# Kernel tuning notes

Measured on AMD Instinct MI355X. Metric: run time of the kernel, lower is better.

## Reference

```python
import jax, jax.numpy as jnp
import numpy as np

D = 512          # d_model
DS = 32          # d_state
EXPAND = 2
HEADDIM = 64
R = 4            # mimo_rank
DIN = EXPAND * D             # 1024 inner dim
H = DIN // HEADDIM           # 16 heads
DFF = ((int(D * 8 / 3) + 7) // 8) * 8  # 1368 SwiGLU hidden
CHUNK = max(1, 64 // R)      # 16
BATCH, SEQ = 4, 512


def setup_inputs() -> dict:
    key = jax.random.key(0)
    ks = jax.random.split(key, 12)
    def w(k, shape, fan):
        return jax.random.normal(k, shape, jnp.float32) / np.float32(np.sqrt(fan))
    return {
        "x": jax.random.normal(ks[0], (BATCH, SEQ, D), jnp.float32),
        "mask": jnp.ones((BATCH, SEQ), jnp.float32),
        "norm1_w": jnp.ones((D,), jnp.float32),
        "norm2_w": jnp.ones((D,), jnp.float32),
        "Wz": w(ks[1], (D, DIN), D),
        "Wx": w(ks[2], (D, DIN), D),
        "Wb": w(ks[3], (D, H * R * DS), D),
        "Wc": w(ks[4], (D, H * R * DS), D),
        "Wdt": w(ks[5], (D, H), D),
        "dt_bias": jnp.zeros((H,), jnp.float32),
        "A_log": jnp.log(jnp.arange(1, H + 1, dtype=jnp.float32)),
        "D_skip": jnp.ones((H,), jnp.float32),
        "Wout": w(ks[6], (DIN, D), DIN),
        "w1": w(ks[7], (D, DFF), D),
        "w2": w(ks[8], (DFF, D), DFF),
        "w3": w(ks[9], (D, DFF), D),
    }


def rmsnorm(x, wgt, eps=1e-6):
    rms = jnp.sqrt(jnp.mean(x * x, axis=-1, keepdims=True) + eps)
    return x / rms * wgt


def ssm_mixer(x, Wz, Wx, Wb, Wc, Wdt, dt_bias, A_log, D_skip, Wout):
    # x: [B, S, D] (already masked)
    B, S, _ = x.shape
    pad = (CHUNK - S % CHUNK) % CHUNK
    if pad > 0:
        x = jnp.pad(x, ((0, 0), (0, pad), (0, 0)))
    Sp = x.shape[1]
    z = x @ Wz                                        # [B,Sp,DIN] gate
    u = (x @ Wx).reshape(B, Sp, H, HEADDIM)           # [B,Sp,H,P]
    Bm = (x @ Wb).reshape(B, Sp, H, R, DS)            # [B,Sp,H,R,N]
    Cm = (x @ Wc).reshape(B, Sp, H, R, DS)
    dt = jax.nn.softplus(x @ Wdt + dt_bias)           # [B,Sp,H]
    a = jnp.exp(dt * (-jnp.exp(A_log)))               # per-step decay [B,Sp,H]
    ud = u * dt[..., None]                            # discretized input

    def step(h, inp):
        a_t, B_t, C_t, ud_t = inp                     # [B,H], [B,H,R,N], [B,H,R,N], [B,H,P]
        h = a_t[:, :, None, None, None] * h + jnp.einsum('bhrn,bhp->bhrnp', B_t, ud_t)
        y = jnp.einsum('bhrn,bhrnp->bhp', C_t, h)
        return h, y

    h0 = jnp.zeros((B, H, R, DS, HEADDIM), x.dtype)
    xs = (a.swapaxes(0, 1), Bm.swapaxes(0, 1), Cm.swapaxes(0, 1), ud.swapaxes(0, 1))
    _, ys = jax.lax.scan(step, h0, xs)                # ys: [Sp,B,H,P]
    y = ys.swapaxes(0, 1) + u * D_skip[None, None, :, None]
    y = y.reshape(B, Sp, DIN) * jax.nn.silu(z)
    y = y @ Wout                                      # [B,Sp,D]
    return y[:, :S]


def reference(x, mask, norm1_w, norm2_w, Wz, Wx, Wb, Wc, Wdt, dt_bias,
              A_log, D_skip, Wout, w1, w2, w3):
    m = mask[..., None]
    xn = rmsnorm(x, norm1_w) * m
    y = ssm_mixer(xn, Wz, Wx, Wb, Wc, Wdt, dt_bias, A_log, D_skip, Wout) * m
    x = x + y
    xn2 = rmsnorm(x, norm2_w)
    x = x + (jax.nn.silu(xn2 @ w1) * (xn2 @ w3)) @ w2
    return x * m
```

## Files before the change

kernel.cpp:

```cpp
#include <hip/hip_runtime.h>
#include <hip/hip_bf16.h>
#include <math.h>

#define Bn 4
#define Sn 512
#define Dn 512
#define DINn 1024
#define Hn 16
#define Pn 64
#define RNn 128
#define DFFn 1368
#define KP2 1408
#define BSn (Bn*Sn)
#define CH 64
#define NCH (Sn/CH)
#define PSTR 6144
#define FPAD 2816
#define NSCAN (Bn*NCH*Hn)
#define NRMS 512

typedef __attribute__((ext_vector_type(8))) short short8;
typedef __attribute__((ext_vector_type(4))) float f32x4;
typedef __attribute__((ext_vector_type(4))) short short4v;

static __device__ __forceinline__ float bf2f(__hip_bfloat16 v){return __bfloat162float(v);}
static __device__ __forceinline__ __hip_bfloat16 f2bf(float v){return __float2bfloat16(v);}
static __device__ __forceinline__ short f2bfs(float v){ __hip_bfloat16 b=f2bf(v); short s; __builtin_memcpy(&s,&b,2); return s; }
static __device__ __forceinline__ float bfs2f(short s){ __hip_bfloat16 b; __builtin_memcpy(&b,&s,2); return bf2f(b); }

static __device__ __forceinline__ int xcd_swz(int bid, int q) {
  return (bid & 7) * q + (bid >> 3);
}

typedef const __attribute__((address_space(1))) unsigned int* gas1_u32p;
typedef __attribute__((address_space(3))) unsigned int* gas3_u32p;
static __device__ __forceinline__ void gl_lds16(const void* g, void* l) {
  __builtin_amdgcn_global_load_lds((gas1_u32p)g, (gas3_u32p)l, 16, 0, 0);
}

struct T8 {
  const float* src[8];
  const float* svec[8];
  __hip_bfloat16* dst[8];
  int Rr[8], Cc[8], RrPad[8], CcPad[8], gw[8];
  int start[9];
};

static __device__ __forceinline__ void transpose_tile(const T8& d, int bid, int t,
                                                      float (*tile)[65]) {
  int i = 0;
#pragma unroll
  for (int k = 1; k < 8; ++k) if (bid >= d.start[k]) i = k;
  int rel = bid - d.start[i];
  int gx = rel % d.gw[i], gy = rel / d.gw[i];
  const float* in = d.src[i];
  const float* sv = d.svec[i];
  __hip_bfloat16* out = d.dst[i];
  int Rr = d.Rr[i], Cc = d.Cc[i], RrPad = d.RrPad[i], CcPad = d.CcPad[i];
  int tx = t & 15, ty = t >> 4;
#pragma unroll
  for (int i4 = 0; i4 < 4; ++i4) {
    int r = gy * 64 + ty + i4 * 16;
    int c0 = gx * 64 + tx * 4;
    f32x4 v = (f32x4){0.f, 0.f, 0.f, 0.f};
    if (r < Rr && c0 + 3 < Cc) v = *(const f32x4*)(in + (size_t)r * Cc + c0);
    tile[ty + i4 * 16][tx * 4 + 0] = v[0];
    tile[ty + i4 * 16][tx * 4 + 1] = v[1];
    tile[ty + i4 * 16][tx * 4 + 2] = v[2];
    tile[ty + i4 * 16][tx * 4 + 3] = v[3];
  }
  __syncthreads();
#pragma unroll
  for (int i4 = 0; i4 < 4; ++i4) {
    int r2 = gx * 64 + ty + i4 * 16;
    int c2 = gy * 64 + tx * 4;
    if (r2 < CcPad && c2 + 3 < RrPad) {
      int k = ty + i4 * 16;
      float s0 = sv ? sv[c2 + 0] : 1.f;
      float s1 = sv ? sv[c2 + 1] : 1.f;
      float s2 = sv ? sv[c2 + 2] : 1.f;
      float s3 = sv ? sv[c2 + 3] : 1.f;
      short4v o;
      o.x = f2bfs(tile[tx * 4 + 0][k] * s0);
      o.y = f2bfs(tile[tx * 4 + 1][k] * s1);
      o.z = f2bfs(tile[tx * 4 + 2][k] * s2);
      o.w = f2bfs(tile[tx * 4 + 3][k] * s3);
      *(short4v*)((short*)out + (size_t)r2 * RrPad + c2) = o;
    }
  }
}

__global__ __launch_bounds__(256) void prep_kernel(
    T8 d, const float* __restrict__ x, const float* __restrict__ w,
    const float* __restrict__ mask, const float* __restrict__ Wdt,
    const float* __restrict__ dtb, const float* __restrict__ Alog,
    __hip_bfloat16* __restrict__ outb, float* __restrict__ dt,
    float* __restrict__ la, float* __restrict__ rs, int tstart) {
  __shared__ __align__(16) char smem[40960];
  int bid = blockIdx.x, t = threadIdx.x;
  if (bid < tstart) {
    transpose_tile(d, bid, t, (float(*)[65])smem);
  } else if (bid - tstart < NRMS) {
    float* wdtS = (float*)smem;
    float* xsS  = (float*)(smem + 32768);
#pragma unroll
    for (int i = 0; i < 8; ++i) {
      int idx = t + i * 256;
      *(f32x4*)&wdtS[idx * 4] = *(const f32x4*)&Wdt[idx * 4];
    }
    __syncthreads();
    int wv = t >> 6, lane = t & 63;
    int row = (bid - tstart) * 4 + wv;
    const float* xr = x + (size_t)row * Dn;
    f32x4 v0 = *(const f32x4*)(xr + lane * 4);
    f32x4 v1 = *(const f32x4*)(xr + 256 + lane * 4);
    float ss = v0[0]*v0[0] + v0[1]*v0[1] + v0[2]*v0[2] + v0[3]*v0[3]
             + v1[0]*v1[0] + v1[1]*v1[1] + v1[2]*v1[2] + v1[3]*v1[3];
#pragma unroll
    for (int o = 32; o > 0; o >>= 1) ss += __shfl_xor(ss, o);
    float sc = rsqrtf(ss * (1.f / Dn) + 1e-6f) * mask[row];
    f32x4 w0 = *(const f32x4*)(w + lane * 4);
    f32x4 w1 = *(const f32x4*)(w + 256 + lane * 4);
    f32x4 o0, o1;
#pragma unroll
    for (int j = 0; j < 4; ++j) { o0[j] = v0[j] * sc * w0[j]; o1[j] = v1[j] * sc * w1[j]; }
    short4v b0, b1;
    b0.x = f2bfs(o0[0]); b0.y = f2bfs(o0[1]); b0.z = f2bfs(o0[2]); b0.w = f2bfs(o0[3]);
    b1.x = f2bfs(o1[0]); b1.y = f2bfs(o1[1]); b1.z = f2bfs(o1[2]); b1.w = f2bfs(o1[3]);
    *(short4v*)((short*)outb + (size_t)row * Dn + lane * 4) = b0;
    *(short4v*)((short*)outb + (size_t)row * Dn + 256 + lane * 4) = b1;
    *(f32x4*)&xsS[wv * 512 + lane * 4] = o0;
    *(f32x4*)&xsS[wv * 512 + 256 + lane * 4] = o1;
    int h = lane >> 2, j = lane & 3;
    float s = 0.f;
#pragma unroll 8
    for (int kk = 0; kk < 128; ++kk) {
      int k = j + kk * 4;
      s = fmaf(xsS[wv * 512 + k], wdtS[k * Hn + h], s);
    }
    s += __shfl_down(s, 2, 4);
    s += __shfl_down(s, 1, 4);
    if (j == 0) {
      float v = s + dtb[h];
      float sp = (v > 20.f) ? v : log1pf(expf(v));
      float Ah = expf(Alog[h]);
      dt[(size_t)row * Hn + h] = sp;
      la[(size_t)row * Hn + h] = -Ah * sp;
    }
  } else {
    *(f32x4*)&rs[t * 8]     = (f32x4){0.f, 0.f, 0.f, 0.f};
    *(f32x4*)&rs[t * 8 + 4] = (f32x4){0.f, 0.f, 0.f, 0.f};
  }
}

__global__ __launch_bounds__(256) void gemm_kernel(
    const __hip_bfloat16* __restrict__ A, const __hip_bfloat16* __restrict__ BT,
    __hip_bfloat16* __restrict__ C, int M, int N, int K) {
  __shared__ short As[2][4096];
  __shared__ short Bs[2][4096];
  int mblocks = M >> 7;
  int wg = xcd_swz(blockIdx.x, (int)gridDim.x >> 3);
  int m0 = (wg % mblocks) * 128, n0 = (wg / mblocks) * 128;
  int t = threadIdx.x;
  int lane = t & 63, wv = t >> 6;
  int wm = (wv & 1) * 64, wn = (wv >> 1) * 64;
  f32x4 acc[4][4];
#pragma unroll
  for (int i = 0; i < 4; ++i)
#pragma unroll
    for (int j = 0; j < 4; ++j) acc[i][j] = (f32x4){0.f, 0.f, 0.f, 0.f};
  const short* Ag = (const short*)A;
  const short* Bg = (const short*)BT;
  int r0 = t >> 2, p = t & 3;
  int q0 = (p - (r0 >> 1)) & 3;
  int r1 = r0 + 64;
  int q1 = (p - (r1 >> 1)) & 3;
  const short* Asrc0 = Ag + (size_t)(m0 + r0) * K + 8 * q0;
  const short* Asrc1 = Ag + (size_t)(m0 + r1) * K + 8 * q1;
  const short* Bsrc0 = Bg + (size_t)(n0 + r0) * K + 8 * q0;
  const short* Bsrc1 = Bg + (size_t)(n0 + r1) * K + 8 * q1;
  int fr = lane & 15, fq = lane >> 4;
  int kTiles = K >> 5;
  auto stage = [&](int buf, int k0) {
    gl_lds16(Asrc0 + k0, &As[buf][wv * 512]);
    gl_lds16(Asrc1 + k0, &As[buf][2048 + wv * 512]);
    gl_lds16(Bsrc0 + k0, &Bs[buf][wv * 512]);
    gl_lds16(Bsrc1 + k0, &Bs[buf][2048 + wv * 512]);
  };
  auto domfma = [&](int buf) {
    short8 af[4], bfr[4];
#pragma unroll
    for (int i = 0; i < 4; ++i) {
      int rr = wm + i * 16 + fr;
      af[i] = *(const short8*)&As[buf][rr * 32 + (((rr >> 1) + fq) & 3) * 8];
    }
#pragma unroll
    for (int i = 0; i < 4; ++i) {
      int rr = wn + i * 16 + fr;
      bfr[i] = *(const short8*)&Bs[buf][rr * 32 + (((rr >> 1) + fq) & 3) * 8];
    }
#pragma unroll
    for (int mi = 0; mi < 4; ++mi)
#pragma unroll
      for (int ni = 0; ni < 4; ++ni)
        acc[mi][ni] = __builtin_amdgcn_mfma_f32_16x16x32_bf16(af[mi], bfr[ni], acc[mi][ni], 0, 0, 0);
  };
  stage(0, 0);
  for (int kt = 0; kt < kTiles; ++kt) {
    int buf = kt & 1;
    __syncthreads();
    if (kt + 1 < kTiles) stage(buf ^ 1, (kt + 1) << 5);
    domfma(buf);
  }
  int fq4 = (lane >> 4) * 4;
#pragma unroll
  for (int mi = 0; mi < 4; ++mi)
#pragma unroll
    for (int ni = 0; ni < 4; ++ni) {
      int col = n0 + wn + ni * 16 + fr;
      if (col < N) {
        int rowb = m0 + wm + mi * 16 + fq4;
#pragma unroll
        for (int r = 0; r < 4; ++r)
          C[(size_t)(rowb + r) * N + col] = f2bf(acc[mi][ni][r]);
      }
    }
}

template <int MODE>
__global__ __launch_bounds__(256) void gemm64_ep_kernel(
    const __hip_bfloat16* __restrict__ A, const __hip_bfloat16* __restrict__ BT,
    const float* __restrict__ aux, const float* __restrict__ mask,
    float* __restrict__ out, __hip_bfloat16* __restrict__ outb,
    float* __restrict__ rs, int M, int N, int K) {
  __shared__ short As[2][64][72];
  __shared__ short Bs[2][64][72];
  int mblocks = M >> 6;
  int wg = xcd_swz(blockIdx.x, (int)gridDim.x >> 3);
  int m0 = (wg % mblocks) * 64, n0 = (wg / mblocks) * 64;
  int t = threadIdx.x;
  int lane = t & 63, wv = t >> 6;
  int wm = (wv & 1) * 32, wn = (wv >> 1) * 32;
  f32x4 acc[2][2];
#pragma unroll
  for (int i = 0; i < 2; ++i)
#pragma unroll
    for (int j = 0; j < 2; ++j) acc[i][j] = (f32x4){0.f, 0.f, 0.f, 0.f};
  const short* Ag = (const short*)A;
  const short* Bg = (const short*)BT;
  int sr = t >> 2;
  int sc = (t & 3) * 16;
  const short* Ap = Ag + (size_t)(m0 + sr) * K + sc;
  const short* Bp = Bg + (size_t)(n0 + sr) * K + sc;
  int fr = lane & 15, fq = (lane >> 4) * 8;
  int kTiles = K >> 6;
  short8 a0A = 0, a1A = 0, b0A = 0, b1A = 0;
  short8 a0B = 0, a1B = 0, b0B = 0, b1B = 0;
  auto loadA = [&](int k0) {
    a0A = *(const short8*)(Ap + k0);
    a1A = *(const short8*)(Ap + k0 + 8);
    b0A = *(const short8*)(Bp + k0);
    b1A = *(const short8*)(Bp + k0 + 8);
  };
  auto loadB = [&](int k0) {
    a0B = *(const short8*)(Ap + k0);
    a1B = *(const short8*)(Ap + k0 + 8);
    b0B = *(const short8*)(Bp + k0);
    b1B = *(const short8*)(Bp + k0 + 8);
  };
  auto storeA = [&](int buf) {
    *(short8*)&As[buf][sr][sc] = a0A;
    *(short8*)&As[buf][sr][sc + 8] = a1A;
    *(short8*)&Bs[buf][sr][sc] = b0A;
    *(short8*)&Bs[buf][sr][sc + 8] = b1A;
  };
  auto storeB = [&](int buf) {
    *(short8*)&As[buf][sr][sc] = a0B;
    *(short8*)&As[buf][sr][sc + 8] = a1B;
    *(short8*)&Bs[buf][sr][sc] = b0B;
    *(short8*)&Bs[buf][sr][sc + 8] = b1B;
  };
  auto mfma = [&](int buf) {
#pragma unroll
    for (int kk = 0; kk < 2; ++kk) {
      short8 af[2], bfr[2];
#pragma unroll
      for (int i = 0; i < 2; ++i) af[i] = *(const short8*)&As[buf][wm + i * 16 + fr][kk * 32 + fq];
#pragma unroll
      for (int i = 0; i < 2; ++i) bfr[i] = *(const short8*)&Bs[buf][wn + i * 16 + fr][kk * 32 + fq];
#pragma unroll
      for (int mi = 0; mi < 2; ++mi)
#pragma unroll
        for (int ni = 0; ni < 2; ++ni)
          acc[mi][ni] = __builtin_amdgcn_mfma_f32_16x16x32_bf16(af[mi], bfr[ni], acc[mi][ni], 0, 0, 0);
    }
  };
  loadA(0);
  storeA(0);
  loadA(64);
  __syncthreads();
  for (int kt = 0; kt < kTiles; kt += 2) {
    storeA(1);
    if (kt + 2 < kTiles) loadB((kt + 2) << 6);
    mfma(0);
    __syncthreads();
    if (kt + 2 < kTiles) storeB(0);
    if (kt + 3 < kTiles) loadA((kt + 3) << 6);
    mfma(1);
    __syncthreads();
  }
  int fq4 = (lane >> 4) * 4;
  float rsum[2][4];
#pragma unroll
  for (int mi = 0; mi < 2; ++mi)
#pragma unroll
    for (int r = 0; r < 4; ++r) rsum[mi][r] = 0.f;
#pragma unroll
  for (int mi = 0; mi < 2; ++mi)
#pragma unroll
    for (int ni = 0; ni < 2; ++ni) {
      int col = n0 + wn + ni * 16 + fr;
#pragma unroll
      for (int r = 0; r < 4; ++r) {
        int row = m0 + wm + mi * 16 + fq4 + r;
        float m = mask[row];
        size_t a = (size_t)row * N + col;
        float v = acc[mi][ni][r];
        if (MODE == 1) {
          float ov = aux[a] + v * m;
          out[a] = ov;
          outb[a] = f2bf(ov);
          rsum[mi][r] += ov * ov;
        } else {
          out[a] = (aux[a] + v) * m;
        }
      }
    }
  if (MODE == 1) {
#pragma unroll
    for (int mi = 0; mi < 2; ++mi)
#pragma unroll
      for (int r = 0; r < 4; ++r) {
        float s = rsum[mi][r];
#pragma unroll
        for (int o = 8; o > 0; o >>= 1) s += __shfl_xor(s, o);
        if ((lane & 15) == 0) {
          int row = m0 + wm + mi * 16 + fq4 + r;
          atomicAdd(&rs[row], s);
        }
      }
  }
}

__global__ __launch_bounds__(256) void gemm64g_kernel(
    const __hip_bfloat16* __restrict__ A, const float* __restrict__ rs,
    const __hip_bfloat16* __restrict__ BT, __hip_bfloat16* __restrict__ G,
    int M, int K) {
  __shared__ short As[2][64][72];
  __shared__ short B1s[2][64][72];
  __shared__ short B3s[2][64][72];
  __shared__ float ssc[64];
  int mblocks = M >> 6;
  int wg = xcd_swz(blockIdx.x, (int)gridDim.x >> 3);
  int m0 = (wg % mblocks) * 64, n0 = (wg / mblocks) * 64;
  int t = threadIdx.x;
  int lane = t & 63, wv = t >> 6;
  int wm = (wv & 1) * 32, wn = (wv >> 1) * 32;
  f32x4 acc1[2][2], acc3[2][2];
#pragma unroll
  for (int i = 0; i < 2; ++i)
#pragma unroll
    for (int j = 0; j < 2; ++j) {
      acc1[i][j] = (f32x4){0.f, 0.f, 0.f, 0.f};
      acc3[i][j] = (f32x4){0.f, 0.f, 0.f, 0.f};
    }
  const short* Ag = (const short*)A;
  const short* Bg = (const short*)BT;
  int sr = t >> 2;
  int sc = (t & 3) * 16;
  const short* Ap  = Ag + (size_t)(m0 + sr) * K + sc;
  const short* B1p = Bg + (size_t)(n0 + sr) * K + sc;
  const short* B3p = Bg + (size_t)(KP2 + n0 + sr) * K + sc;
  int fr = lane & 15, fq = (lane >> 4) * 8;
  int kTiles = K >> 6;
  if (t < 64) ssc[t] = rsqrtf(rs[m0 + t] * (1.f / Dn) + 1e-6f);
  short8 a0A = 0, a1A = 0, c0A = 0, c1A = 0, d0A = 0, d1A = 0;
  short8 a0B = 0, a1B = 0, c0B = 0, c1B = 0, d0B = 0, d1B = 0;
  auto loadA = [&](int k0) {
    a0A = *(const short8*)(Ap + k0);
    a1A = *(const short8*)(Ap + k0 + 8);
    c0A = *(const short8*)(B1p + k0);
    c1A = *(const short8*)(B1p + k0 + 8);
    d0A = *(const short8*)(B3p + k0);
    d1A = *(const short8*)(B3p + k0 + 8);
  };
  auto loadB = [&](int k0) {
    a0B = *(const short8*)(Ap + k0);
    a1B = *(const short8*)(Ap + k0 + 8);
    c0B = *(const short8*)(B1p + k0);
    c1B = *(const short8*)(B1p + k0 + 8);
    d0B = *(const short8*)(B3p + k0);
    d1B = *(const short8*)(B3p + k0 + 8);
  };
  auto storeA = [&](int buf) {
    *(short8*)&As[buf][sr][sc] = a0A;
    *(short8*)&As[buf][sr][sc + 8] = a1A;
    *(short8*)&B1s[buf][sr][sc] = c0A;
    *(short8*)&B1s[buf][sr][sc + 8] = c1A;
    *(short8*)&B3s[buf][sr][sc] = d0A;
    *(short8*)&B3s[buf][sr][sc + 8] = d1A;
  };
  auto storeB = [&](int buf) {
    *(short8*)&As[buf][sr][sc] = a0B;
    *(short8*)&As[buf][sr][sc + 8] = a1B;
    *(short8*)&B1s[buf][sr][sc] = c0B;
    *(short8*)&B1s[buf][sr][sc + 8] = c1B;
    *(short8*)&B3s[buf][sr][sc] = d0B;
    *(short8*)&B3s[buf][sr][sc + 8] = d1B;
  };
  auto mfma = [&](int buf) {
#pragma unroll
    for (int kk = 0; kk < 2; ++kk) {
      short8 af[2], b1f[2], b3f[2];
#pragma unroll
      for (int i = 0; i < 2; ++i) af[i]  = *(const short8*)&As[buf][wm + i * 16 + fr][kk * 32 + fq];
#pragma unroll
      for (int i = 0; i < 2; ++i) b1f[i] = *(const short8*)&B1s[buf][wn + i * 16 + fr][kk * 32 + fq];
#pragma unroll
      for (int i = 0; i < 2; ++i) b3f[i] = *(const short8*)&B3s[buf][wn + i * 16 + fr][kk * 32 + fq];
#pragma unroll
      for (int mi = 0; mi < 2; ++mi)
#pragma unroll
        for (int ni = 0; ni < 2; ++ni) {
          acc1[mi][ni] = __builtin_amdgcn_mfma_f32_16x16x32_bf16(af[mi], b1f[ni], acc1[mi][ni], 0, 0, 0);
          acc3[mi][ni] = __builtin_amdgcn_mfma_f32_16x16x32_bf16(af[mi], b3f[ni], acc3[mi][ni], 0, 0, 0);
        }
    }
  };
  loadA(0);
  storeA(0);
  loadA(64);
  __syncthreads();
  for (int kt = 0; kt < kTiles; kt += 2) {
    storeA(1);
    if (kt + 2 < kTiles) loadB((kt + 2) << 6);
    mfma(0);
    __syncthreads();
    if (kt + 2 < kTiles) storeB(0);
    if (kt + 3 < kTiles) loadA((kt + 3) << 6);
    mfma(1);
    __syncthreads();
  }
  int fq4 = (lane >> 4) * 4;
#pragma unroll
  for (int mi = 0; mi < 2; ++mi)
#pragma unroll
    for (int ni = 0; ni < 2; ++ni) {
      int col = n0 + wn + ni * 16 + fr;
#pragma unroll
      for (int r = 0; r < 4; ++r) {
        int rloc = wm + mi * 16 + fq4 + r;
        float scl = ssc[rloc];
        float h1v = acc1[mi][ni][r] * scl;
        float sil = h1v / (1.f + __expf(-h1v));
        float g = sil * (acc3[mi][ni][r] * scl);
        G[(size_t)(m0 + rloc) * KP2 + col] = f2bf(g);
      }
    }
}

__global__ __launch_bounds__(256) void chunk_state_kernel(
    const __hip_bfloat16* __restrict__ P, const float* __restrict__ dt,
    const float* __restrict__ la, __hip_bfloat16* __restrict__ Sbuf,
    float* __restrict__ ecL) {
  int id = blockIdx.x;
  int h = id & 15, c = (id >> 4) & 7, b = id >> 7;
  int t = threadIdx.x, lane = t & 63, wv = t >> 6;
  __shared__ __align__(16) char smem[45824];
  short* sB   = (short*)smem;
  short* sUD  = (short*)(smem + 17408);
  short* sBwT = (short*)(smem + 26624);
  float* scum = (float*)(smem + 45056);
  float* sws  = scum + 64;
  float* sdt  = sws + 64;
  int row0 = b * Sn + c * CH;
  const short* Pb = (const short*)P;
#pragma unroll
  for (int i = 0; i < 4; ++i) {
    int idx = t + i * 256;
    int r = idx >> 4, kk = (idx & 15) * 8;
    *(short8*)&sB[r * 136 + kk] = *(const short8*)(Pb + (size_t)(row0 + r) * PSTR + 2048 + h * 128 + kk);
  }
  if (t < 64) { sdt[t] = dt[(size_t)(row0 + t) * Hn + h]; scum[t] = la[(size_t)(row0 + t) * Hn + h]; }
  __syncthreads();
  if (wv == 0) {
    float v = scum[lane];
#pragma unroll
    for (int o = 1; o < 64; o <<= 1) { float n = __shfl_up(v, o); if (lane >= o) v += n; }
    float c63 = __shfl(v, 63);
    sws[lane] = __expf(c63 - v);
    if (lane == 0) ecL[(b * NCH + c) * Hn + h] = __expf(c63);
  }
#pragma unroll
  for (int i = 0; i < 2; ++i) {
    int idx = t + i * 256;
    int s = idx >> 3, pc = (idx & 7) * 8;
    short8 uv = *(const short8*)(Pb + (size_t)(row0 + s) * PSTR + 1024 + h * 64 + pc);
    float dv = sdt[s];
#pragma unroll
    for (int j = 0; j < 8; ++j) sUD[(pc + j) * 72 + s] = f2bfs(bfs2f(uv[j]) * dv);
  }
  __syncthreads();
#pragma unroll
  for (int i = 0; i < 32; ++i) {
    int idx = t + i * 256;
    int rn = idx >> 6, s = idx & 63;
    sBwT[rn * 72 + s] = f2bfs(bfs2f(sB[s * 136 + rn]) * sws[s]);
  }
  __syncthreads();
  int fr = lane & 15, fq = (lane >> 4) * 8, q4 = (lane >> 4) * 4;
#pragma unroll
  for (int mt0 = 0; mt0 < 2; ++mt0) {
    int mt = wv * 2 + mt0;
    short8 ab[2];
#pragma unroll
    for (int k = 0; k < 2; ++k) ab[k] = *(short8*)&sBwT[(16 * mt + fr) * 72 + k * 32 + fq];
#pragma unroll
    for (int j = 0; j < 4; ++j) {
      f32x4 acc = (f32x4){0.f, 0.f, 0.f, 0.f};
#pragma unroll
      for (int k = 0; k < 2; ++k) {
        short8 bf = *(short8*)&sUD[(16 * j + fr) * 72 + k * 32 + fq];
        acc = __builtin_amdgcn_mfma_f32_16x16x32_bf16(ab[k], bf, acc, 0, 0, 0);
      }
      int pp = 16 * j + fr;
      int rn0 = 16 * mt + q4;
      short4v o;
      o.x = f2bfs(acc[0]); o.y = f2bfs(acc[1]); o.z = f2bfs(acc[2]); o.w = f2bfs(acc[3]);
      *(short4v*)&((short*)Sbuf)[((size_t)((b * NCH + c) * Hn + h) * 64 + pp) * 128 + rn0] = o;
    }
  }
}

__global__ __launch_bounds__(256) void intra_inter_gate_kernel(
    const __hip_bfloat16* __restrict__ P, const float* __restrict__ dt,
    const float* __restrict__ la, const __hip_bfloat16* __restrict__ Sbuf,
    const float* __restrict__ ecL, const float* __restrict__ Dsk,
    __hip_bfloat16* __restrict__ y2b) {
  int id = blockIdx.x;
  int h = id & 15, c = (id >> 4) & 7, b = id >> 7;
  int t = threadIdx.x, lane = t & 63, wv = t >> 6;
  __shared__ __align__(16) char smem[54016];
  short* sCB = (short*)smem;
  short* sB  = (short*)(smem + 17408);
  short* sUD = (short*)(smem + 34816);
  short* sG  = (short*)(smem + 44032);
  short* sHt = (short*)(smem + 34816);
  short* sz  = sB;
  short* su  = sB + 4096;
  float* scum = (float*)(smem + 53248);
  float* sdt  = scum + 64;
  int row0 = b * Sn + c * CH;
  const short* Pb = (const short*)P;
#pragma unroll
  for (int i = 0; i < 4; ++i) {
    int idx = t + i * 256;
    int r = idx >> 4, kk = (idx & 15) * 8;
    *(short8*)&sCB[r * 136 + kk] = *(const short8*)(Pb + (size_t)(row0 + r) * PSTR + 4096 + h * 128 + kk);
    *(short8*)&sB [r * 136 + kk] = *(const short8*)(Pb + (size_t)(row0 + r) * PSTR + 2048 + h * 128 + kk);
  }
  if (t < 64) { sdt[t] = dt[(size_t)(row0 + t) * Hn + h]; scum[t] = la[(size_t)(row0 + t) * Hn + h]; }
  __syncthreads();
  if (wv == 0) {
    float v = scum[lane];
#pragma unroll
    for (int o = 1; o < 64; o <<= 1) { float n = __shfl_up(v, o); if (lane >= o) v += n; }
    scum[lane] = v;
  }
#pragma unroll
  for (int i = 0; i < 2; ++i) {
    int idx = t + i * 256;
    int s = idx >> 3, pc = (idx & 7) * 8;
    short8 uv = *(const short8*)(Pb + (size_t)(row0 + s) * PSTR + 1024 + h * 64 + pc);
    float dv = sdt[s];
#pragma unroll
    for (int j = 0; j < 8; ++j) sUD[(pc + j) * 72 + s] = f2bfs(bfs2f(uv[j]) * dv);
  }
  __syncthreads();
  int fr = lane & 15, fq = (lane >> 4) * 8, q4 = (lane >> 4) * 4;
  {
    short8 af[4];
#pragma unroll
    for (int k = 0; k < 4; ++k) af[k] = *(short8*)&sCB[(16 * wv + fr) * 136 + k * 32 + fq];
#pragma unroll
    for (int j = 0; j < 4; ++j) {
      f32x4 acc = (f32x4){0.f, 0.f, 0.f, 0.f};
#pragma unroll
      for (int k = 0; k < 4; ++k) {
        short8 bf = *(short8*)&sB[(16 * j + fr) * 136 + k * 32 + fq];
        acc = __builtin_amdgcn_mfma_f32_16x16x32_bf16(af[k], bf, acc, 0, 0, 0);
      }
      int ss = 16 * j + fr;
      float cs = scum[ss];
#pragma unroll
      for (int r = 0; r < 4; ++r) {
        int tt = 16 * wv + q4 + r;
        float w = (ss <= tt) ? __expf(scum[tt] - cs) : 0.f;
        sG[tt * 72 + ss] = f2bfs(acc[r] * w);
      }
    }
  }
  __syncthreads();
  f32x4 ysr[4];
  {
    short8 ag[2];
#pragma unroll
    for (int k = 0; k < 2; ++k) ag[k] = *(short8*)&sG[(16 * wv + fr) * 72 + k * 32 + fq];
#pragma unroll
    for (int j = 0; j < 4; ++j) {
      f32x4 acc = (f32x4){0.f, 0.f, 0.f, 0.f};
#pragma unroll
      for (int k = 0; k < 2; ++k) {
        short8 bf = *(short8*)&sUD[(16 * j + fr) * 72 + k * 32 + fq];
        acc = __builtin_amdgcn_mfma_f32_16x16x32_bf16(ag[k], bf, acc, 0, 0, 0);
      }
      ysr[j] = acc;
    }
  }
#pragma unroll
  for (int i = 0; i < 2; ++i) {
    int idx = t + i * 256;
    int r = idx >> 3, pc = (idx & 7) * 8;
    *(short8*)&sz[r * 64 + pc] = *(const short8*)(Pb + (size_t)(row0 + r) * PSTR + h * 64 + pc);
    *(short8*)&su[r * 64 + pc] = *(const short8*)(Pb + (size_t)(row0 + r) * PSTR + 1024 + h * 64 + pc);
  }
  float hacc[32];
#pragma unroll
  for (int jj = 0; jj < 32; ++jj) hacc[jj] = 0.f;
  if (c > 0) {
    const short* Sb = (const short*)Sbuf;
    float wrun = 1.f;
    for (int cp = c - 1; cp >= 0; --cp) {
      size_t base = ((size_t)((b * NCH + cp) * Hn + h)) * 8192 + (size_t)t * 32;
#pragma unroll
      for (int v4 = 0; v4 < 4; ++v4) {
        short8 sv = *(const short8*)(Sb + base + v4 * 8);
#pragma unroll
        for (int jj = 0; jj < 8; ++jj)
          hacc[v4 * 8 + jj] = fmaf(wrun, bfs2f(sv[jj]), hacc[v4 * 8 + jj]);
      }
      wrun *= ecL[(size_t)((b * NCH + cp) * Hn + h)];
    }
  }
  __syncthreads();
  if (c > 0) {
    int pp = t >> 2, rn0 = (t & 3) * 32;
#pragma unroll
    for (int v4 = 0; v4 < 4; ++v4) {
      short8 o;
#pragma unroll
      for (int jj = 0; jj < 8; ++jj) o[jj] = f2bfs(hacc[v4 * 8 + jj]);
      *(short8*)&sHt[pp * 136 + rn0 + v4 * 8] = o;
    }
  }
  __syncthreads();
  f32x4 acc[4];
#pragma unroll
  for (int j = 0; j < 4; ++j) acc[j] = (f32x4){0.f, 0.f, 0.f, 0.f};
  if (c > 0) {
    short8 af[4];
#pragma unroll
    for (int k = 0; k < 4; ++k) af[k] = *(short8*)&sCB[(16 * wv + fr) * 136 + k * 32 + fq];
#pragma unroll
    for (int j = 0; j < 4; ++j)
#pragma unroll
      for (int k = 0; k < 4; ++k) {
        short8 bf = *(short8*)&sHt[(16 * j + fr) * 136 + k * 32 + fq];
        acc[j] = __builtin_amdgcn_mfma_f32_16x16x32_bf16(af[k], bf, acc[j], 0, 0, 0);
      }
  }
  float dsk = Dsk[h];
#pragma unroll
  for (int j = 0; j < 4; ++j) {
    int col = 16 * j + fr;
#pragma unroll
    for (int r = 0; r < 4; ++r) {
      int tt = 16 * wv + q4 + r;
      size_t a = (size_t)(row0 + tt) * DINn + h * 64 + col;
      float val = ysr[j][r];
      if (c > 0) val += __expf(scum[tt]) * acc[j][r];
      float uu = bfs2f(su[tt * 64 + col]);
      float zz = bfs2f(sz[tt * 64 + col]);
      float sil = zz / (1.f + __expf(-zz));
      y2b[a] = f2bf((val + uu * dsk) * sil);
    }
  }
}

extern "C" void kernel_launch(void* const* d_in, const int* in_sizes, int n_in,
                              void* d_out, int out_size, void* d_ws, size_t ws_size,
                              hipStream_t stream) {
  const float* x    = (const float*)d_in[0];
  const float* mask = (const float*)d_in[1];
  const float* n1w  = (const float*)d_in[2];
  const float* n2w  = (const float*)d_in[3];
  const float* Wz   = (const float*)d_in[4];
  const float* Wx   = (const float*)d_in[5];
  const float* Wb   = (const float*)d_in[6];
  const float* Wc   = (const float*)d_in[7];
  const float* Wdt  = (const float*)d_in[8];
  const float* dtb  = (const float*)d_in[9];
  const float* Alog = (const float*)d_in[10];
  const float* Dsk  = (const float*)d_in[11];
  const float* Wout = (const float*)d_in[12];
  const float* w1   = (const float*)d_in[13];
  const float* w2   = (const float*)d_in[14];
  const float* w3   = (const float*)d_in[15];

  char* ws = (char*)d_ws;
  size_t off = 0;
  auto alloc = [&](size_t bytes) {
    char* p = ws + off;
    off += (bytes + 255) & ~(size_t)255;
    return p;
  };
  __hip_bfloat16* xnb = (__hip_bfloat16*)alloc((size_t)BSn * Dn * 2);
  __hip_bfloat16* P = (__hip_bfloat16*)alloc((size_t)BSn * PSTR * 2);
  float* dt  = (float*)alloc((size_t)BSn * Hn * 4);
  float* la  = (float*)alloc((size_t)BSn * Hn * 4);
  float* ecL = (float*)alloc((size_t)Bn * NCH * Hn * 4);
  float* rs  = (float*)alloc((size_t)BSn * 4);
  __hip_bfloat16* WallT = (__hip_bfloat16*)alloc((size_t)PSTR * Dn * 2);
  __hip_bfloat16* WoutT = (__hip_bfloat16*)alloc((size_t)Dn * DINn * 2);
  __hip_bfloat16* w13T  = (__hip_bfloat16*)alloc((size_t)FPAD * Dn * 2);
  __hip_bfloat16* w2T   = (__hip_bfloat16*)alloc((size_t)Dn * KP2 * 2);
  char* arena = alloc(23200000);
  __hip_bfloat16* Sbuf = (__hip_bfloat16*)arena;
  __hip_bfloat16* y2b  = (__hip_bfloat16*)(arena + 16777216);
  float* xres          = (float*)arena;
  __hip_bfloat16* gatedb = (__hip_bfloat16*)(arena + 4194304);
  __hip_bfloat16* xresb  = (__hip_bfloat16*)(arena + 20971520);

  T8 td;
  for (int i = 0; i < 8; ++i) td.svec[i] = nullptr;
  td.src[0] = Wz;   td.dst[0] = WallT;                      td.Rr[0] = 512;  td.Cc[0] = 1024; td.RrPad[0] = 512;  td.CcPad[0] = 1024;
  td.src[1] = Wx;   td.dst[1] = WallT + (size_t)1024 * 512; td.Rr[1] = 512;  td.Cc[1] = 1024; td.RrPad[1] = 512;  td.CcPad[1] = 1024;
  td.src[2] = Wb;   td.dst[2] = WallT + (size_t)2048 * 512; td.Rr[2] = 512;  td.Cc[2] = 2048; td.RrPad[2] = 512;  td.CcPad[2] = 2048;
  td.src[3] = Wc;   td.dst[3] = WallT + (size_t)4096 * 512; td.Rr[3] = 512;  td.Cc[3] = 2048; td.RrPad[3] = 512;  td.CcPad[3] = 2048;
  td.src[4] = Wout; td.dst[4] = WoutT;                      td.Rr[4] = 1024; td.Cc[4] = 512;  td.RrPad[4] = 1024; td.CcPad[4] = 512;
  td.src[5] = w1;   td.dst[5] = w13T;                       td.Rr[5] = 512;  td.Cc[5] = 1368; td.RrPad[5] = 512;  td.CcPad[5] = KP2;
  td.src[6] = w3;   td.dst[6] = w13T + (size_t)KP2 * 512;   td.Rr[6] = 512;  td.Cc[6] = 1368; td.RrPad[6] = 512;  td.CcPad[6] = KP2;
  td.src[7] = w2;   td.dst[7] = w2T;                        td.Rr[7] = 1368; td.Cc[7] = 512;  td.RrPad[7] = KP2;  td.CcPad[7] = 512;
  td.svec[5] = n2w;
  td.svec[6] = n2w;
  int tot = 0;
  for (int i = 0; i < 8; ++i) {
    td.gw[i] = (td.CcPad[i] + 63) / 64;
    int gh = (td.RrPad[i] + 63) / 64;
    td.start[i] = tot;
    tot += td.gw[i] * gh;
  }
  td.start[8] = tot;

  prep_kernel<<<tot + NRMS + 1, 256, 0, stream>>>(td, x, n1w, mask, Wdt, dtb, Alog, xnb, dt, la, rs, tot);
  gemm_kernel<<<16 * 48, 256, 0, stream>>>(xnb, WallT, P, BSn, PSTR, Dn);
  chunk_state_kernel<<<NSCAN, 256, 0, stream>>>(P, dt, la, Sbuf, ecL);
  intra_inter_gate_kernel<<<NSCAN, 256, 0, stream>>>(P, dt, la, Sbuf, ecL, Dsk, y2b);
  gemm64_ep_kernel<1><<<32 * 8, 256, 0, stream>>>(y2b, WoutT, x, mask, xres, xresb, rs, BSn, Dn, DINn);
  gemm64g_kernel<<<32 * (KP2 / 64), 256, 0, stream>>>(xresb, rs, w13T, gatedb, BSn, Dn);
  gemm64_ep_kernel<2><<<32 * 8, 256, 0, stream>>>(gatedb, w2T, xres, mask, (float*)d_out, nullptr, rs, BSn, Dn, KP2);
}
```

Before: 182.9 us.

## Stage GEMM tiles with direct global-to-LDS loads and swizzled layout

The epilogue GEMM and the fused SwiGLU gate GEMM now copy A/B tiles straight from global memory into LDS with `gl_lds16`, replacing the register round-trip. The padded 72-wide LDS rows become a dense 64-wide layout, with a rotation swizzle on the 8-element chunk index to avoid bank conflicts. The double-buffered loop drops from two barriers per pair of k-tiles to one barrier per tile, and prefetches the next tile before the MFMAs on the current one. This frees registers and removes LDS store instructions. The risk is correctness of the async copy ordering, since it relies on the helper or the barrier to wait for the loads to complete.

```diff
diff --git a/kernel.cpp b/kernel.cpp
--- a/kernel.cpp
+++ b/kernel.cpp
@@ -233,8 +233,8 @@
     const float* __restrict__ aux, const float* __restrict__ mask,
     float* __restrict__ out, __hip_bfloat16* __restrict__ outb,
     float* __restrict__ rs, int M, int N, int K) {
-  __shared__ short As[2][64][72];
-  __shared__ short Bs[2][64][72];
+  __shared__ short As[2][4096];
+  __shared__ short Bs[2][4096];
   int mblocks = M >> 6;
   int wg = xcd_swz(blockIdx.x, (int)gridDim.x >> 3);
   int m0 = (wg % mblocks) * 64, n0 = (wg / mblocks) * 64;
@@ -248,46 +248,36 @@
     for (int j = 0; j < 2; ++j) acc[i][j] = (f32x4){0.f, 0.f, 0.f, 0.f};
   const short* Ag = (const short*)A;
   const short* Bg = (const short*)BT;
-  int sr = t >> 2;
-  int sc = (t & 3) * 16;
-  const short* Ap = Ag + (size_t)(m0 + sr) * K + sc;
-  const short* Bp = Bg + (size_t)(n0 + sr) * K + sc;
-  int fr = lane & 15, fq = (lane >> 4) * 8;
+  int r0 = t >> 3, p = t & 7;
+  int q0 = (p - r0) & 7;
+  int r1 = r0 + 32;
+  int q1 = (p - r1) & 7;
+  const short* Asrc0 = Ag + (size_t)(m0 + r0) * K + q0 * 8;
+  const short* Asrc1 = Ag + (size_t)(m0 + r1) * K + q1 * 8;
+  const short* Bsrc0 = Bg + (size_t)(n0 + r0) * K + q0 * 8;
+  const short* Bsrc1 = Bg + (size_t)(n0 + r1) * K + q1 * 8;
+  int fr = lane & 15, fh = lane >> 4;
   int kTiles = K >> 6;
-  short8 a0A = 0, a1A = 0, b0A = 0, b1A = 0;
-  short8 a0B = 0, a1B = 0, b0B = 0, b1B = 0;
-  auto loadA = [&](int k0) {
-    a0A = *(const short8*)(Ap + k0);
-    a1A = *(const short8*)(Ap + k0 + 8);
-    b0A = *(const short8*)(Bp + k0);
-    b1A = *(const short8*)(Bp + k0 + 8);
+  auto stage = [&](int buf, int k0) {
+    gl_lds16(Asrc0 + k0, &As[buf][wv * 512]);
+    gl_lds16(Asrc1 + k0, &As[buf][2048 + wv * 512]);
+    gl_lds16(Bsrc0 + k0, &Bs[buf][wv * 512]);
+    gl_lds16(Bsrc1 + k0, &Bs[buf][2048 + wv * 512]);
   };
-  auto loadB = [&](int k0) {
-    a0B = *(const short8*)(Ap + k0);
-    a1B = *(const short8*)(Ap + k0 + 8);
-    b0B = *(const short8*)(Bp + k0);
-    b1B = *(const short8*)(Bp + k0 + 8);
-  };
-  auto storeA = [&](int buf) {
-    *(short8*)&As[buf][sr][sc] = a0A;
-    *(short8*)&As[buf][sr][sc + 8] = a1A;
-    *(short8*)&Bs[buf][sr][sc] = b0A;
-    *(short8*)&Bs[buf][sr][sc + 8] = b1A;
-  };
-  auto storeB = [&](int buf) {
-    *(short8*)&As[buf][sr][sc] = a0B;
-    *(short8*)&As[buf][sr][sc + 8] = a1B;
-    *(short8*)&Bs[buf][sr][sc] = b0B;
-    *(short8*)&Bs[buf][sr][sc + 8] = b1B;
-  };
-  auto mfma = [&](int buf) {
+  auto domfma = [&](int buf) {
 #pragma unroll
     for (int kk = 0; kk < 2; ++kk) {
       short8 af[2], bfr[2];
 #pragma unroll
-      for (int i = 0; i < 2; ++i) af[i] = *(const short8*)&As[buf][wm + i * 16 + fr][kk * 32 + fq];
-#pragma unroll
-      for (int i = 0; i < 2; ++i) bfr[i] = *(const short8*)&Bs[buf][wn + i * 16 + fr][kk * 32 + fq];
+      for (int i = 0; i < 2; ++i) {
+        int rr = wm + i * 16 + fr;
+        af[i] = *(const short8*)&As[buf][rr * 64 + (((rr + kk * 4 + fh) & 7) * 8)];
+      }
+#pragma unroll
+      for (int i = 0; i < 2; ++i) {
+        int rr = wn + i * 16 + fr;
+        bfr[i] = *(const short8*)&Bs[buf][rr * 64 + (((rr + kk * 4 + fh) & 7) * 8)];
+      }
 #pragma unroll
       for (int mi = 0; mi < 2; ++mi)
 #pragma unroll
@@ -295,19 +285,12 @@
           acc[mi][ni] = __builtin_amdgcn_mfma_f32_16x16x32_bf16(af[mi], bfr[ni], acc[mi][ni], 0, 0, 0);
     }
   };
-  loadA(0);
-  storeA(0);
-  loadA(64);
-  __syncthreads();
-  for (int kt = 0; kt < kTiles; kt += 2) {
-    storeA(1);
-    if (kt + 2 < kTiles) loadB((kt + 2) << 6);
-    mfma(0);
+  stage(0, 0);
+  for (int kt = 0; kt < kTiles; ++kt) {
+    int buf = kt & 1;
     __syncthreads();
-    if (kt + 2 < kTiles) storeB(0);
-    if (kt + 3 < kTiles) loadA((kt + 3) << 6);
-    mfma(1);
-    __syncthreads();
+    if (kt + 1 < kTiles) stage(buf ^ 1, (kt + 1) << 6);
+    domfma(buf);
   }
   int fq4 = (lane >> 4) * 4;
   float rsum[2][4];
@@ -356,9 +339,9 @@
     const __hip_bfloat16* __restrict__ A, const float* __restrict__ rs,
     const __hip_bfloat16* __restrict__ BT, __hip_bfloat16* __restrict__ G,
     int M, int K) {
-  __shared__ short As[2][64][72];
-  __shared__ short B1s[2][64][72];
-  __shared__ short B3s[2][64][72];
+  __shared__ short As[2][4096];
+  __shared__ short B1s[2][4096];
+  __shared__ short B3s[2][4096];
   __shared__ float ssc[64];
   int mblocks = M >> 6;
   int wg = xcd_swz(blockIdx.x, (int)gridDim.x >> 3);
@@ -376,58 +359,43 @@
     }
   const short* Ag = (const short*)A;
   const short* Bg = (const short*)BT;
-  int sr = t >> 2;
-  int sc = (t & 3) * 16;
-  const short* Ap  = Ag + (size_t)(m0 + sr) * K + sc;
-  const short* B1p = Bg + (size_t)(n0 + sr) * K + sc;
-  const short* B3p = Bg + (size_t)(KP2 + n0 + sr) * K + sc;
-  int fr = lane & 15, fq = (lane >> 4) * 8;
+  int r0 = t >> 3, p = t & 7;
+  int q0 = (p - r0) & 7;
+  int r1 = r0 + 32;
+  int q1 = (p - r1) & 7;
+  const short* Asrc0  = Ag + (size_t)(m0 + r0) * K + q0 * 8;
+  const short* Asrc1  = Ag + (size_t)(m0 + r1) * K + q1 * 8;
+  const short* B1src0 = Bg + (size_t)(n0 + r0) * K + q0 * 8;
+  const short* B1src1 = Bg + (size_t)(n0 + r1) * K + q1 * 8;
+  const short* B3src0 = Bg + (size_t)(KP2 + n0 + r0) * K + q0 * 8;
+  const short* B3src1 = Bg + (size_t)(KP2 + n0 + r1) * K + q1 * 8;
+  int fr = lane & 15, fh = lane >> 4;
   int kTiles = K >> 6;
   if (t < 64) ssc[t] = rsqrtf(rs[m0 + t] * (1.f / Dn) + 1e-6f);
-  short8 a0A = 0, a1A = 0, c0A = 0, c1A = 0, d0A = 0, d1A = 0;
-  short8 a0B = 0, a1B = 0, c0B = 0, c1B = 0, d0B = 0, d1B = 0;
-  auto loadA = [&](int k0) {
-    a0A = *(const short8*)(Ap + k0);
-    a1A = *(const short8*)(Ap + k0 + 8);
-    c0A = *(const short8*)(B1p + k0);
-    c1A = *(const short8*)(B1p + k0 + 8);
-    d0A = *(const short8*)(B3p + k0);
-    d1A = *(const short8*)(B3p + k0 + 8);
+  auto stage = [&](int buf, int k0) {
+    gl_lds16(Asrc0 + k0, &As[buf][wv * 512]);
+    gl_lds16(Asrc1 + k0, &As[buf][2048 + wv * 512]);
+    gl_lds16(B1src0 + k0, &B1s[buf][wv * 512]);
+    gl_lds16(B1src1 + k0, &B1s[buf][2048 + wv * 512]);
+    gl_lds16(B3src0 + k0, &B3s[buf][wv * 512]);
+    gl_lds16(B3src1 + k0, &B3s[buf][2048 + wv * 512]);
   };
-  auto loadB = [&](int k0) {
-    a0B = *(const short8*)(Ap + k0);
-    a1B = *(const short8*)(Ap + k0 + 8);
-    c0B = *(const short8*)(B1p + k0);
-    c1B = *(const short8*)(B1p + k0 + 8);
-    d0B = *(const short8*)(B3p + k0);
-    d1B = *(const short8*)(B3p + k0 + 8);
-  };
-  auto storeA = [&](int buf) {
-    *(short8*)&As[buf][sr][sc] = a0A;
-    *(short8*)&As[buf][sr][sc + 8] = a1A;
-    *(short8*)&B1s[buf][sr][sc] = c0A;
-    *(short8*)&B1s[buf][sr][sc + 8] = c1A;
-    *(short8*)&B3s[buf][sr][sc] = d0A;
-    *(short8*)&B3s[buf][sr][sc + 8] = d1A;
-  };
-  auto storeB = [&](int buf) {
-    *(short8*)&As[buf][sr][sc] = a0B;
-    *(short8*)&As[buf][sr][sc + 8] = a1B;
-    *(short8*)&B1s[buf][sr][sc] = c0B;
-    *(short8*)&B1s[buf][sr][sc + 8] = c1B;
-    *(short8*)&B3s[buf][sr][sc] = d0B;
-    *(short8*)&B3s[buf][sr][sc + 8] = d1B;
-  };
-  auto mfma = [&](int buf) {
+  auto domfma = [&](int buf) {
 #pragma unroll
     for (int kk = 0; kk < 2; ++kk) {
       short8 af[2], b1f[2], b3f[2];
 #pragma unroll
-      for (int i = 0; i < 2; ++i) af[i]  = *(const short8*)&As[buf][wm + i * 16 + fr][kk * 32 + fq];
-#pragma unroll
-      for (int i = 0; i < 2; ++i) b1f[i] = *(const short8*)&B1s[buf][wn + i * 16 + fr][kk * 32 + fq];
-#pragma unroll
-      for (int i = 0; i < 2; ++i) b3f[i] = *(const short8*)&B3s[buf][wn + i * 16 + fr][kk * 32 + fq];
+      for (int i = 0; i < 2; ++i) {
+        int rr = wm + i * 16 + fr;
+        af[i] = *(const short8*)&As[buf][rr * 64 + (((rr + kk * 4 + fh) & 7) * 8)];
+      }
+#pragma unroll
+      for (int i = 0; i < 2; ++i) {
+        int rr = wn + i * 16 + fr;
+        int so = rr * 64 + (((rr + kk * 4 + fh) & 7) * 8);
+        b1f[i] = *(const short8*)&B1s[buf][so];
+        b3f[i] = *(const short8*)&B3s[buf][so];
+      }
 #pragma unroll
       for (int mi = 0; mi < 2; ++mi)
 #pragma unroll
@@ -437,19 +405,12 @@
         }
     }
   };
-  loadA(0);
-  storeA(0);
-  loadA(64);
-  __syncthreads();
-  for (int kt = 0; kt < kTiles; kt += 2) {
-    storeA(1);
-    if (kt + 2 < kTiles) loadB((kt + 2) << 6);
-    mfma(0);
+  stage(0, 0);
+  for (int kt = 0; kt < kTiles; ++kt) {
+    int buf = kt & 1;
     __syncthreads();
-    if (kt + 2 < kTiles) storeB(0);
-    if (kt + 3 < kTiles) loadA((kt + 3) << 6);
-    mfma(1);
-    __syncthreads();
+    if (kt + 1 < kTiles) stage(buf ^ 1, (kt + 1) << 6);
+    domfma(buf);
   }
   int fq4 = (lane >> 4) * 4;
 #pragma unroll
```

Result: slower. 189.9 us (+3.8%).
